# Kernel tuning notes

Measured on AMD Instinct MI355X. Metric: run time of the kernel, lower is better.

## Reference

```python
import jax, jax.numpy as jnp
import numpy as np


def _rnn_scan(x_tbi, h0, Wih, Whh, bih, bhh):
    # x_tbi: [T,B,I], h0: [B,H]. PyTorch nn.RNN cell: h = tanh(x@Wih^T + bih + h@Whh^T + bhh)
    def step(h, xt):
        h_new = jnp.tanh(xt @ Wih.T + bih + h @ Whh.T + bhh)
        return h_new, h_new
    h_last, hs = jax.lax.scan(step, h0, x_tbi)
    return h_last, hs


def setup_inputs() -> dict:
    key = jax.random.key(0)
    ks = jax.random.split(key, 12)
    B, T, I, H, O = 4096, 64, 3, 128, 3
    s = 1.0 / np.sqrt(H)
    d = {
        "x": jax.random.normal(ks[0], (B, T, I), dtype=jnp.float32),
        "enc_Wih": jax.random.uniform(ks[1], (H, I), jnp.float32, -s, s),
        "enc_Whh": jax.random.uniform(ks[2], (H, H), jnp.float32, -s, s),
        "enc_bih": jax.random.uniform(ks[3], (H,), jnp.float32, -s, s),
        "enc_bhh": jax.random.uniform(ks[4], (H,), jnp.float32, -s, s),
        "dec_Wih": jax.random.uniform(ks[5], (H, O), jnp.float32, -s, s),
        "dec_Whh": jax.random.uniform(ks[6], (H, H), jnp.float32, -s, s),
        "dec_bih": jax.random.uniform(ks[7], (H,), jnp.float32, -s, s),
        "dec_bhh": jax.random.uniform(ks[8], (H,), jnp.float32, -s, s),
        "fc_W": jax.random.uniform(ks[9], (O, H), jnp.float32, -s, s),
        "fc_b": jax.random.uniform(ks[10], (O,), jnp.float32, -s, s),
        "pred_len": 32,
    }
    return d


def reference(x, enc_Wih, enc_Whh, enc_bih, enc_bhh,
              dec_Wih, dec_Whh, dec_bih, dec_bhh, fc_W, fc_b, pred_len):
    B, T, _ = x.shape
    H = enc_Whh.shape[0]
    h0 = jnp.zeros((B, H), dtype=x.dtype)
    # Encoder over LOOK_BACK steps
    h, _ = _rnn_scan(jnp.swapaxes(x, 0, 1), h0, enc_Wih, enc_Whh, enc_bih, enc_bhh)
    dec_in0 = x[:, -1, :]  # [B,O]

    def step(carry, _):
        h, inp = carry
        h_new = jnp.tanh(inp @ dec_Wih.T + dec_bih + h @ dec_Whh.T + dec_bhh)
        pred = h_new @ fc_W.T + fc_b
        return (h_new, pred), pred

    _, preds = jax.lax.scan(step, (h, dec_in0), None, length=pred_len)
    out = jnp.swapaxes(preds, 0, 1)  # [B, pred_len, O]
    if pred_len == 1:
        return out[:, 0, :]
    return out
```

## Files before the change

kernel.cpp:

```cpp
#include <hip/hip_runtime.h>

typedef short short8 __attribute__((ext_vector_type(8)));
typedef float f32x4 __attribute__((ext_vector_type(4)));

#define H 128
#define NB 16
#define TSTEPS 64
#define PRED 32
#define XSTRIDE 260


static __device__ __forceinline__ unsigned short bf16_rne(float f) {
  unsigned u = __builtin_bit_cast(unsigned, f);
  u += 0x7fffu + ((u >> 16) & 1u);
  return (unsigned short)(u >> 16);
}
static __device__ __forceinline__ float bf16_f(unsigned short s) {
  unsigned u = ((unsigned)s) << 16;
  return __builtin_bit_cast(float, u);
}
static __device__ __forceinline__ float tanh_fast(float v) {
  v = fminf(9.0f, fmaxf(-9.0f, v));
  float e = __expf(2.0f * v);
  return __fdividef(e - 1.0f, e + 1.0f);
}

static __device__ __forceinline__ void split_frag(const f32x4& a, const f32x4& b,
                                                  short8& hi, short8& lo) {
  #pragma unroll
  for (int e = 0; e < 4; ++e) {
    unsigned short h1 = bf16_rne(a[e]);
    hi[e] = (short)h1;
    lo[e] = (short)bf16_rne(a[e] - bf16_f(h1));
    unsigned short h2 = bf16_rne(b[e]);
    hi[e + 4] = (short)h2;
    lo[e + 4] = (short)bf16_rne(b[e] - bf16_f(h2));
  }
}

__global__ __launch_bounds__(512, 2) void traj_kernel(
    const float* __restrict__ x,
    const float* __restrict__ eWih, const float* __restrict__ eWhh,
    const float* __restrict__ ebih, const float* __restrict__ ebhh,
    const float* __restrict__ dWih, const float* __restrict__ dWhh,
    const float* __restrict__ dbih, const float* __restrict__ dbhh,
    const float* __restrict__ fcW, const float* __restrict__ fcb,
    float* __restrict__ out)
{
  __shared__ __align__(16) float x_lds[NB * XSTRIDE];
  __shared__ __align__(16) short h_hi0[NB * H], h_lo0[NB * H];
  __shared__ __align__(16) short h_hi1[NB * H], h_lo1[NB * H];
  __shared__ float inp_lds[NB][4];

  const int tid = threadIdx.x;
  const int lane = tid & 63;
  const int w = tid >> 6;
  const int l4 = lane >> 4;
  const int ln = lane & 15;
  const int r0 = blockIdx.x * NB;
  const int jj = w * 16 + ln;

  #pragma unroll
  for (int s = 0; s < 6; ++s) {
    int flat = tid + s * 512;
    int r = flat / 192;
    int rem = flat - r * 192;
    int t = rem / 3;
    int i = rem - t * 3;
    x_lds[r * XSTRIDE + t * 4 + i] = x[(size_t)r0 * 192 + flat];
  }
  #pragma unroll
  for (int s = 0; s < 4; ++s) {
    h_hi0[tid + s * 512] = 0;
    h_lo0[tid + s * 512] = 0;
  }

  short8 whi[4], wlo[4];
  #pragma unroll
  for (int kt = 0; kt < 4; ++kt) {
    const float* p = eWhh + jj * H + kt * 32 + l4 * 8;
    split_frag(*(const f32x4*)p, *(const f32x4*)(p + 4), whi[kt], wlo[kt]);
  }
  float bias = ebih[jj] + ebhh[jj];
  float wi[3];
  #pragma unroll
  for (int i = 0; i < 3; ++i) wi[i] = eWih[jj * 3 + i];

  int roff[4];
  #pragma unroll
  for (int kt = 0; kt < 4; ++kt)
    roff[kt] = ln * H + ((((kt << 2) + l4) ^ ln) << 3);
  int wo[4], xb[4];
  #pragma unroll
  for (int reg = 0; reg < 4; ++reg) {
    const int r = l4 * 4 + reg;
    wo[reg] = r * H + (((jj >> 3) ^ r) << 3) + (jj & 7);
    xb[reg] = r * XSTRIDE;
  }

  auto load_frags = [&](const short* __restrict__ hh, const short* __restrict__ hl,
                        short8* ah, short8* al) {
    #pragma unroll
    for (int kt = 0; kt < 4; ++kt) {
      ah[kt] = *(const short8*)&hh[roff[kt]];
      al[kt] = *(const short8*)&hl[roff[kt]];
    }
  };
  auto rnn_core = [&](const short8* ah, const short8* al, f32x4 acc0,
                      short* __restrict__ wh, short* __restrict__ wl) {
    f32x4 accb = {0.f, 0.f, 0.f, 0.f};
    f32x4 accc = {0.f, 0.f, 0.f, 0.f};
    #pragma unroll
    for (int kt = 0; kt < 4; ++kt) {
      acc0 = __builtin_amdgcn_mfma_f32_16x16x32_bf16(ah[kt], whi[kt], acc0, 0, 0, 0);
      accb = __builtin_amdgcn_mfma_f32_16x16x32_bf16(ah[kt], wlo[kt], accb, 0, 0, 0);
      accc = __builtin_amdgcn_mfma_f32_16x16x32_bf16(al[kt], whi[kt], accc, 0, 0, 0);
    }
    #pragma unroll
    for (int reg = 0; reg < 4; ++reg) {
      float v = tanh_fast(acc0[reg] + accb[reg] + accc[reg]);
      unsigned short p = bf16_rne(v);
      wh[wo[reg]] = (short)p;
      wl[wo[reg]] = (short)bf16_rne(v - bf16_f(p));
    }
  };

  __syncthreads();

  for (int t = 0; t < TSTEPS; t += 2) {
    {
      short8 ah[4], al[4];
      load_frags(h_hi0, h_lo0, ah, al);
      f32x4 a;
      #pragma unroll
      for (int reg = 0; reg < 4; ++reg) {
        const f32x4 xv = *(const f32x4*)&x_lds[xb[reg] + t * 4];
        a[reg] = bias + wi[0] * xv[0] + wi[1] * xv[1] + wi[2] * xv[2];
      }
      rnn_core(ah, al, a, h_hi1, h_lo1);
    }
    __syncthreads();
    {
      short8 ah[4], al[4];
      load_frags(h_hi1, h_lo1, ah, al);
      f32x4 a;
      #pragma unroll
      for (int reg = 0; reg < 4; ++reg) {
        const f32x4 xv = *(const f32x4*)&x_lds[xb[reg] + (t + 1) * 4];
        a[reg] = bias + wi[0] * xv[0] + wi[1] * xv[1] + wi[2] * xv[2];
      }
      rnn_core(ah, al, a, h_hi0, h_lo0);
    }
    __syncthreads();
  }

  #pragma unroll
  for (int kt = 0; kt < 4; ++kt) {
    const float* p = dWhh + jj * H + kt * 32 + l4 * 8;
    split_frag(*(const f32x4*)p, *(const f32x4*)(p + 4), whi[kt], wlo[kt]);
  }
  bias = dbih[jj] + dbhh[jj];
  #pragma unroll
  for (int i = 0; i < 3; ++i) wi[i] = dWih[jj * 3 + i];

  short8 fhi[4];
  #pragma unroll
  for (int kt = 0; kt < 4; ++kt) {
    f32x4 a = {0.f, 0.f, 0.f, 0.f}, b = {0.f, 0.f, 0.f, 0.f};
    if (ln < 3) {
      const float* p = fcW + ln * H + kt * 32 + l4 * 8;
      a = *(const f32x4*)p;
      b = *(const f32x4*)(p + 4);
    }
    short8 hi;
    #pragma unroll
    for (int e = 0; e < 4; ++e) {
      hi[e] = (short)bf16_rne(a[e]);
      hi[e + 4] = (short)bf16_rne(b[e]);
    }
    fhi[kt] = hi;
  }
  const float fcbl = (ln < 3) ? fcb[ln] : 0.f;

  if (tid < 48) {
    int r = tid / 3, i = tid - 3 * (tid / 3);
    inp_lds[r][i] = x_lds[r * XSTRIDE + 63 * 4 + i];
  }
  __syncthreads();

  {
    short8 ah[4], al[4];
    load_frags(h_hi0, h_lo0, ah, al);
    f32x4 a;
    #pragma unroll
    for (int reg = 0; reg < 4; ++reg) {
      const int r = l4 * 4 + reg;
      a[reg] = bias + wi[0] * inp_lds[r][0] + wi[1] * inp_lds[r][1]
                    + wi[2] * inp_lds[r][2];
    }
    rnn_core(ah, al, a, h_hi1, h_lo1);
  }
  __syncthreads();

  #pragma unroll
  for (int kt = 0; kt < 4; ++kt) {
    const int kb = kt * 32 + l4 * 8;
    f32x4 a = *(const f32x4*)(dWhh + jj * H + kb);
    f32x4 b = *(const f32x4*)(dWhh + jj * H + kb + 4);
    #pragma unroll
    for (int o = 0; o < 3; ++o) {
      const f32x4 fa = *(const f32x4*)(fcW + o * H + kb);
      const f32x4 fb = *(const f32x4*)(fcW + o * H + kb + 4);
      #pragma unroll
      for (int e = 0; e < 4; ++e) {
        a[e] += wi[o] * fa[e];
        b[e] += wi[o] * fb[e];
      }
    }
    split_frag(a, b, whi[kt], wlo[kt]);
  }
  const float biasp = bias + wi[0] * fcb[0] + wi[1] * fcb[1] + wi[2] * fcb[2];
  const f32x4 accd = {biasp, biasp, biasp, biasp};

  const short* rdh = h_hi1; const short* rdl = h_lo1;
  short* wrh = h_hi0;       short* wrl = h_lo0;
  for (int s = 1; s < PRED; ++s) {
    short8 ah[4], al[4];
    load_frags(rdh, rdl, ah, al);
    rnn_core(ah, al, accd, wrh, wrl);
    if (w == (s & 7)) {
      f32x4 f0 = {0.f, 0.f, 0.f, 0.f};
      f32x4 f1 = {0.f, 0.f, 0.f, 0.f};
      #pragma unroll
      for (int kt = 0; kt < 4; ++kt) {
        f0 = __builtin_amdgcn_mfma_f32_16x16x32_bf16(ah[kt], fhi[kt], f0, 0, 0, 0);
        f1 = __builtin_amdgcn_mfma_f32_16x16x32_bf16(al[kt], fhi[kt], f1, 0, 0, 0);
      }
      if (ln < 3) {
        #pragma unroll
        for (int reg = 0; reg < 4; ++reg)
          out[((size_t)(r0 + l4 * 4 + reg) * PRED + (s - 1)) * 3 + ln] =
              f0[reg] + f1[reg] + fcbl;
      }
    }
    __syncthreads();
    const short* th = rdh; rdh = wrh; wrh = (short*)th;
    const short* tl = rdl; rdl = wrl; wrl = (short*)tl;
  }
  if (w == 0) {
    short8 ah[4], al[4];
    load_frags(rdh, rdl, ah, al);
    f32x4 f0 = {0.f, 0.f, 0.f, 0.f};
    f32x4 f1 = {0.f, 0.f, 0.f, 0.f};
    #pragma unroll
    for (int kt = 0; kt < 4; ++kt) {
      f0 = __builtin_amdgcn_mfma_f32_16x16x32_bf16(ah[kt], fhi[kt], f0, 0, 0, 0);
      f1 = __builtin_amdgcn_mfma_f32_16x16x32_bf16(al[kt], fhi[kt], f1, 0, 0, 0);
    }
    if (ln < 3) {
      #pragma unroll
      for (int reg = 0; reg < 4; ++reg)
        out[((size_t)(r0 + l4 * 4 + reg) * PRED + (PRED - 1)) * 3 + ln] =
            f0[reg] + f1[reg] + fcbl;
    }
  }
}

extern "C" void kernel_launch(void* const* d_in, const int* in_sizes, int n_in,
                              void* d_out, int out_size, void* d_ws, size_t ws_size,
                              hipStream_t stream) {
  (void)in_sizes; (void)n_in; (void)out_size; (void)d_ws; (void)ws_size;
  const float* x    = (const float*)d_in[0];
  const float* eWih = (const float*)d_in[1];
  const float* eWhh = (const float*)d_in[2];
  const float* ebih = (const float*)d_in[3];
  const float* ebhh = (const float*)d_in[4];
  const float* dWih = (const float*)d_in[5];
  const float* dWhh = (const float*)d_in[6];
  const float* dbih = (const float*)d_in[7];
  const float* dbhh = (const float*)d_in[8];
  const float* fcW  = (const float*)d_in[9];
  const float* fcb  = (const float*)d_in[10];
  float* out = (float*)d_out;
  traj_kernel<<<dim3(256), dim3(512), 0, stream>>>(
      x, eWih, eWhh, ebih, ebhh, dWih, dWhh, dbih, dbhh, fcW, fcb, out);
}
```

Baseline: 151.4 us.

## Halve batch rows per block and give each wave two output column tiles

Result: slower. 167.0 us (+10.3%).

```diff
diff --git a/kernel.cpp b/kernel.cpp
--- a/kernel.cpp
+++ b/kernel.cpp
@@ -4,7 +4,7 @@
 typedef float f32x4 __attribute__((ext_vector_type(4)));
 
 #define H 128
-#define NB 16
+#define NB 8
 #define TSTEPS 64
 #define PRED 32
 #define XSTRIDE 260
@@ -38,7 +38,7 @@
   }
 }
 
-__global__ __launch_bounds__(512, 2) void traj_kernel(
+__global__ __launch_bounds__(256, 2) void traj_kernel(
     const float* __restrict__ x,
     const float* __restrict__ eWih, const float* __restrict__ eWhh,
     const float* __restrict__ ebih, const float* __restrict__ ebhh,
@@ -47,10 +47,10 @@
     const float* __restrict__ fcW, const float* __restrict__ fcb,
     float* __restrict__ out)
 {
-  __shared__ __align__(16) float x_lds[NB * XSTRIDE];
-  __shared__ __align__(16) short h_hi0[NB * H], h_lo0[NB * H];
-  __shared__ __align__(16) short h_hi1[NB * H], h_lo1[NB * H];
-  __shared__ float inp_lds[NB][4];
+  __shared__ __align__(16) float x_lds[16 * XSTRIDE];
+  __shared__ __align__(16) short h_hi0[16 * H], h_lo0[16 * H];
+  __shared__ __align__(16) short h_hi1[16 * H], h_lo1[16 * H];
+  __shared__ float inp_lds[16][4];
 
   const int tid = threadIdx.x;
   const int lane = tid & 63;
@@ -58,43 +58,51 @@
   const int l4 = lane >> 4;
   const int ln = lane & 15;
   const int r0 = blockIdx.x * NB;
-  const int jj = w * 16 + ln;
-
-  #pragma unroll
-  for (int s = 0; s < 6; ++s) {
-    int flat = tid + s * 512;
+  const int jj0 = w * 32 + ln;
+  const int jj1 = jj0 + 16;
+
+  #pragma unroll
+  for (int s = 0; s < 12; ++s) {
+    int flat = tid + s * 256;
     int r = flat / 192;
     int rem = flat - r * 192;
     int t = rem / 3;
     int i = rem - t * 3;
-    x_lds[r * XSTRIDE + t * 4 + i] = x[(size_t)r0 * 192 + flat];
-  }
-  #pragma unroll
-  for (int s = 0; s < 4; ++s) {
-    h_hi0[tid + s * 512] = 0;
-    h_lo0[tid + s * 512] = 0;
-  }
-
-  short8 whi[4], wlo[4];
-  #pragma unroll
-  for (int kt = 0; kt < 4; ++kt) {
-    const float* p = eWhh + jj * H + kt * 32 + l4 * 8;
-    split_frag(*(const f32x4*)p, *(const f32x4*)(p + 4), whi[kt], wlo[kt]);
-  }
-  float bias = ebih[jj] + ebhh[jj];
-  float wi[3];
-  #pragma unroll
-  for (int i = 0; i < 3; ++i) wi[i] = eWih[jj * 3 + i];
+    int g = (r >> 2) * 2 + (r & 1);
+    x_lds[r * XSTRIDE + t * 4 + i] = x[(size_t)(r0 + g) * 192 + rem];
+  }
+  #pragma unroll
+  for (int s = 0; s < 8; ++s) {
+    h_hi0[tid + s * 256] = 0; h_hi1[tid + s * 256] = 0;
+    h_lo0[tid + s * 256] = 0; h_lo1[tid + s * 256] = 0;
+  }
+
+  short8 whi[2][4], wlo[2][4];
+  #pragma unroll
+  for (int ct = 0; ct < 2; ++ct) {
+    const int j = ct ? jj1 : jj0;
+    #pragma unroll
+    for (int kt = 0; kt < 4; ++kt) {
+      const float* p = eWhh + j * H + kt * 32 + l4 * 8;
+      split_frag(*(const f32x4*)p, *(const f32x4*)(p + 4), whi[ct][kt], wlo[ct][kt]);
+    }
+  }
+  float bias0 = ebih[jj0] + ebhh[jj0];
+  float bias1 = ebih[jj1] + ebhh[jj1];
+  float wi0[3], wi1[3];
+  #pragma unroll
+  for (int i = 0; i < 3; ++i) { wi0[i] = eWih[jj0 * 3 + i]; wi1[i] = eWih[jj1 * 3 + i]; }
 
   int roff[4];
   #pragma unroll
   for (int kt = 0; kt < 4; ++kt)
     roff[kt] = ln * H + ((((kt << 2) + l4) ^ ln) << 3);
-  int wo[4], xb[4];
-  #pragma unroll
-  for (int reg = 0; reg < 4; ++reg) {
+  int wo0[2], wo1[2], xb[2];
+  #pragma unroll
+  for (int reg = 0; reg < 2; ++reg) {
     const int r = l4 * 4 + reg;
-    wo[reg] = r * H + (((jj >> 3) ^ r) << 3) + (jj & 7);
+    wo0[reg] = r * H + (((jj0 >> 3) ^ r) << 3) + (jj0 & 7);
+    wo1[reg] = r * H + (((jj1 >> 3) ^ r) << 3) + (jj1 & 7);
     xb[reg] = r * XSTRIDE;
   }
 
@@ -106,22 +114,29 @@
       al[kt] = *(const short8*)&hl[roff[kt]];
     }
   };
-  auto rnn_core = [&](const short8* ah, const short8* al, f32x4 acc0,
+  auto rnn_core = [&](const short8* ah, const short8* al, f32x4 a0, f32x4 a1,
                       short* __restrict__ wh, short* __restrict__ wl) {
-    f32x4 accb = {0.f, 0.f, 0.f, 0.f};
-    f32x4 accc = {0.f, 0.f, 0.f, 0.f};
-    #pragma unroll
-    for (int kt = 0; kt < 4; ++kt) {
-      acc0 = __builtin_amdgcn_mfma_f32_16x16x32_bf16(ah[kt], whi[kt], acc0, 0, 0, 0);
-      accb = __builtin_amdgcn_mfma_f32_16x16x32_bf16(ah[kt], wlo[kt], accb, 0, 0, 0);
-      accc = __builtin_amdgcn_mfma_f32_16x16x32_bf16(al[kt], whi[kt], accc, 0, 0, 0);
-    }
-    #pragma unroll
-    for (int reg = 0; reg < 4; ++reg) {
-      float v = tanh_fast(acc0[reg] + accb[reg] + accc[reg]);
-      unsigned short p = bf16_rne(v);
-      wh[wo[reg]] = (short)p;
-      wl[wo[reg]] = (short)bf16_rne(v - bf16_f(p));
+    f32x4 b0 = {0.f, 0.f, 0.f, 0.f}, b1 = {0.f, 0.f, 0.f, 0.f};
+    f32x4 c0 = {0.f, 0.f, 0.f, 0.f}, c1 = {0.f, 0.f, 0.f, 0.f};
+    #pragma unroll
+    for (int kt = 0; kt < 4; ++kt) {
+      a0 = __builtin_amdgcn_mfma_f32_16x16x32_bf16(ah[kt], whi[0][kt], a0, 0, 0, 0);
+      a1 = __builtin_amdgcn_mfma_f32_16x16x32_bf16(ah[kt], whi[1][kt], a1, 0, 0, 0);
+      b0 = __builtin_amdgcn_mfma_f32_16x16x32_bf16(ah[kt], wlo[0][kt], b0, 0, 0, 0);
+      b1 = __builtin_amdgcn_mfma_f32_16x16x32_bf16(ah[kt], wlo[1][kt], b1, 0, 0, 0);
+      c0 = __builtin_amdgcn_mfma_f32_16x16x32_bf16(al[kt], whi[0][kt], c0, 0, 0, 0);
+      c1 = __builtin_amdgcn_mfma_f32_16x16x32_bf16(al[kt], whi[1][kt], c1, 0, 0, 0);
+    }
+    #pragma unroll
+    for (int reg = 0; reg < 2; ++reg) {
+      float v0 = tanh_fast(a0[reg] + b0[reg] + c0[reg]);
+      float v1 = tanh_fast(a1[reg] + b1[reg] + c1[reg]);
+      unsigned short p0 = bf16_rne(v0);
+      unsigned short p1 = bf16_rne(v1);
+      wh[wo0[reg]] = (short)p0;
+      wl[wo0[reg]] = (short)bf16_rne(v0 - bf16_f(p0));
+      wh[wo1[reg]] = (short)p1;
+      wl[wo1[reg]] = (short)bf16_rne(v1 - bf16_f(p1));
     }
   };
 
@@ -131,37 +146,44 @@
     {
       short8 ah[4], al[4];
       load_frags(h_hi0, h_lo0, ah, al);
-      f32x4 a;
-      #pragma unroll
-      for (int reg = 0; reg < 4; ++reg) {
+      f32x4 a0 = {0.f, 0.f, bias0, bias0}, a1 = {0.f, 0.f, bias1, bias1};
+      #pragma unroll
+      for (int reg = 0; reg < 2; ++reg) {
         const f32x4 xv = *(const f32x4*)&x_lds[xb[reg] + t * 4];
-        a[reg] = bias + wi[0] * xv[0] + wi[1] * xv[1] + wi[2] * xv[2];
-      }
-      rnn_core(ah, al, a, h_hi1, h_lo1);
+        a0[reg] = bias0 + wi0[0] * xv[0] + wi0[1] * xv[1] + wi0[2] * xv[2];
+        a1[reg] = bias1 + wi1[0] * xv[0] + wi1[1] * xv[1] + wi1[2] * xv[2];
+      }
+      rnn_core(ah, al, a0, a1, h_hi1, h_lo1);
     }
     __syncthreads();
     {
       short8 ah[4], al[4];
       load_frags(h_hi1, h_lo1, ah, al);
-      f32x4 a;
-      #pragma unroll
-      for (int reg = 0; reg < 4; ++reg) {
+      f32x4 a0 = {0.f, 0.f, bias0, bias0}, a1 = {0.f, 0.f, bias1, bias1};
+      #pragma unroll
+      for (int reg = 0; reg < 2; ++reg) {
         const f32x4 xv = *(const f32x4*)&x_lds[xb[reg] + (t + 1) * 4];
-        a[reg] = bias + wi[0] * xv[0] + wi[1] * xv[1] + wi[2] * xv[2];
-      }
-      rnn_core(ah, al, a, h_hi0, h_lo0);
+        a0[reg] = bias0 + wi0[0] * xv[0] + wi0[1] * xv[1] + wi0[2] * xv[2];
+        a1[reg] = bias1 + wi1[0] * xv[0] + wi1[1] * xv[1] + wi1[2] * xv[2];
+      }
+      rnn_core(ah, al, a0, a1, h_hi0, h_lo0);
     }
     __syncthreads();
   }
 
   #pragma unroll
-  for (int kt = 0; kt < 4; ++kt) {
-    const float* p = dWhh + jj * H + kt * 32 + l4 * 8;
-    split_frag(*(const f32x4*)p, *(const f32x4*)(p + 4), whi[kt], wlo[kt]);
-  }
-  bias = dbih[jj] + dbhh[jj];
-  #pragma unroll
-  for (int i = 0; i < 3; ++i) wi[i] = dWih[jj * 3 + i];
+  for (int ct = 0; ct < 2; ++ct) {
+    const int j = ct ? jj1 : jj0;
+    #pragma unroll
+    for (int kt = 0; kt < 4; ++kt) {
+      const float* p = dWhh + j * H + kt * 32 + l4 * 8;
+      split_frag(*(const f32x4*)p, *(const f32x4*)(p + 4), whi[ct][kt], wlo[ct][kt]);
+    }
+  }
+  bias0 = dbih[jj0] + dbhh[jj0];
+  bias1 = dbih[jj1] + dbhh[jj1];
+  #pragma unroll
+  for (int i = 0; i < 3; ++i) { wi0[i] = dWih[jj0 * 3 + i]; wi1[i] = dWih[jj1 * 3 + i]; }
 
   short8 fhi[4];
   #pragma unroll
@@ -191,56 +213,65 @@
   {
     short8 ah[4], al[4];
     load_frags(h_hi0, h_lo0, ah, al);
-    f32x4 a;
-    #pragma unroll
-    for (int reg = 0; reg < 4; ++reg) {
+    f32x4 a0 = {0.f, 0.f, bias0, bias0}, a1 = {0.f, 0.f, bias1, bias1};
+    #pragma unroll
+    for (int reg = 0; reg < 2; ++reg) {
       const int r = l4 * 4 + reg;
-      a[reg] = bias + wi[0] * inp_lds[r][0] + wi[1] * inp_lds[r][1]
-                    + wi[2] * inp_lds[r][2];
-    }
-    rnn_core(ah, al, a, h_hi1, h_lo1);
+      a0[reg] = bias0 + wi0[0] * inp_lds[r][0] + wi0[1] * inp_lds[r][1]
+                      + wi0[2] * inp_lds[r][2];
+      a1[reg] = bias1 + wi1[0] * inp_lds[r][0] + wi1[1] * inp_lds[r][1]
+                      + wi1[2] * inp_lds[r][2];
+    }
+    rnn_core(ah, al, a0, a1, h_hi1, h_lo1);
   }
   __syncthreads();
 
   #pragma unroll
-  for (int kt = 0; kt < 4; ++kt) {
-    const int kb = kt * 32 + l4 * 8;
-    f32x4 a = *(const f32x4*)(dWhh + jj * H + kb);
-    f32x4 b = *(const f32x4*)(dWhh + jj * H + kb + 4);
-    #pragma unroll
-    for (int o = 0; o < 3; ++o) {
-      const f32x4 fa = *(const f32x4*)(fcW + o * H + kb);
-      const f32x4 fb = *(const f32x4*)(fcW + o * H + kb + 4);
-      #pragma unroll
-      for (int e = 0; e < 4; ++e) {
-        a[e] += wi[o] * fa[e];
-        b[e] += wi[o] * fb[e];
-      }
-    }
-    split_frag(a, b, whi[kt], wlo[kt]);
-  }
-  const float biasp = bias + wi[0] * fcb[0] + wi[1] * fcb[1] + wi[2] * fcb[2];
-  const f32x4 accd = {biasp, biasp, biasp, biasp};
+  for (int ct = 0; ct < 2; ++ct) {
+    const int j = ct ? jj1 : jj0;
+    const float* wip = ct ? wi1 : wi0;
+    #pragma unroll
+    for (int kt = 0; kt < 4; ++kt) {
+      const int kb = kt * 32 + l4 * 8;
+      f32x4 a = *(const f32x4*)(dWhh + j * H + kb);
+      f32x4 b = *(const f32x4*)(dWhh + j * H + kb + 4);
+      #pragma unroll
+      for (int o = 0; o < 3; ++o) {
+        const f32x4 fa = *(const f32x4*)(fcW + o * H + kb);
+        const f32x4 fb = *(const f32x4*)(fcW + o * H + kb + 4);
+        #pragma unroll
+        for (int e = 0; e < 4; ++e) {
+          a[e] += wip[o] * fa[e];
+          b[e] += wip[o] * fb[e];
+        }
+      }
+      split_frag(a, b, whi[ct][kt], wlo[ct][kt]);
+    }
+  }
+  const float biasp0 = bias0 + wi0[0] * fcb[0] + wi0[1] * fcb[1] + wi0[2] * fcb[2];
+  const float biasp1 = bias1 + wi1[0] * fcb[0] + wi1[1] * fcb[1] + wi1[2] * fcb[2];
+  const f32x4 accd0 = {biasp0, biasp0, biasp0, biasp0};
+  const f32x4 accd1 = {biasp1, biasp1, biasp1, biasp1};
 
   const short* rdh = h_hi1; const short* rdl = h_lo1;
   short* wrh = h_hi0;       short* wrl = h_lo0;
   for (int s = 1; s < PRED; ++s) {
     short8 ah[4], al[4];
     load_frags(rdh, rdl, ah, al);
-    rnn_core(ah, al, accd, wrh, wrl);
-    if (w == (s & 7)) {
-      f32x4 f0 = {0.f, 0.f, 0.f, 0.f};
-      f32x4 f1 = {0.f, 0.f, 0.f, 0.f};
+    rnn_core(ah, al, accd0, accd1, wrh, wrl);
+    if (w == (s & 3)) {
+      f32x4 p0 = {0.f, 0.f, 0.f, 0.f};
+      f32x4 p1 = {0.f, 0.f, 0.f, 0.f};
       #pragma unroll
       for (int kt = 0; kt < 4; ++kt) {
-        f0 = __builtin_amdgcn_mfma_f32_16x16x32_bf16(ah[kt], fhi[kt], f0, 0, 0, 0);
-        f1 = __builtin_amdgcn_mfma_f32_16x16x32_bf16(al[kt], fhi[kt], f1, 0, 0, 0);
+        p0 = __builtin_amdgcn_mfma_f32_16x16x32_bf16(ah[kt], fhi[kt], p0, 0, 0, 0);
+        p1 = __builtin_amdgcn_mfma_f32_16x16x32_bf16(al[kt], fhi[kt], p1, 0, 0, 0);
       }
       if (ln < 3) {
         #pragma unroll
-        for (int reg = 0; reg < 4; ++reg)
-          out[((size_t)(r0 + l4 * 4 + reg) * PRED + (s - 1)) * 3 + ln] =
-              f0[reg] + f1[reg] + fcbl;
+        for (int reg = 0; reg < 2; ++reg)
+          out[((size_t)(r0 + l4 * 2 + reg) * PRED + (s - 1)) * 3 + ln] =
+              p0[reg] + p1[reg] + fcbl;
       }
     }
     __syncthreads();
@@ -250,18 +281,18 @@
   if (w == 0) {
     short8 ah[4], al[4];
     load_frags(rdh, rdl, ah, al);
-    f32x4 f0 = {0.f, 0.f, 0.f, 0.f};
-    f32x4 f1 = {0.f, 0.f, 0.f, 0.f};
-    #pragma unroll
-    for (int kt = 0; kt < 4; ++kt) {
-      f0 = __builtin_amdgcn_mfma_f32_16x16x32_bf16(ah[kt], fhi[kt], f0, 0, 0, 0);
-      f1 = __builtin_amdgcn_mfma_f32_16x16x32_bf16(al[kt], fhi[kt], f1, 0, 0, 0);
+    f32x4 p0 = {0.f, 0.f, 0.f, 0.f};
+    f32x4 p1 = {0.f, 0.f, 0.f, 0.f};
+    #pragma unroll
+    for (int kt = 0; kt < 4; ++kt) {
+      p0 = __builtin_amdgcn_mfma_f32_16x16x32_bf16(ah[kt], fhi[kt], p0, 0, 0, 0);
+      p1 = __builtin_amdgcn_mfma_f32_16x16x32_bf16(al[kt], fhi[kt], p1, 0, 0, 0);
     }
     if (ln < 3) {
       #pragma unroll
-      for (int reg = 0; reg < 4; ++reg)
-        out[((size_t)(r0 + l4 * 4 + reg) * PRED + (PRED - 1)) * 3 + ln] =
-            f0[reg] + f1[reg] + fcbl;
+      for (int reg = 0; reg < 2; ++reg)
+        out[((size_t)(r0 + l4 * 2 + reg) * PRED + (PRED - 1)) * 3 + ln] =
+            p0[reg] + p1[reg] + fcbl;
     }
   }
 }
@@ -282,6 +313,6 @@
   const float* fcW  = (const float*)d_in[9];
   const float* fcb  = (const float*)d_in[10];
   float* out = (float*)d_out;
-  traj_kernel<<<dim3(256), dim3(512), 0, stream>>>(
+  traj_kernel<<<dim3(512), dim3(256), 0, stream>>>(
       x, eWih, eWhh, ebih, ebhh, dWih, dWhh, dbih, dbhh, fcW, fcb, out);
 }
```

## Drop low-half hidden state split and stream x from global registers

Applied to the files above, without the earlier changes.

Result: faster. 136.9 us (-9.6%).

```diff
diff --git a/kernel.cpp b/kernel.cpp
--- a/kernel.cpp
+++ b/kernel.cpp
@@ -7,7 +7,6 @@
 #define NB 16
 #define TSTEPS 64
 #define PRED 32
-#define XSTRIDE 260
 
 
 static __device__ __forceinline__ unsigned short bf16_rne(float f) {
@@ -47,10 +46,8 @@
     const float* __restrict__ fcW, const float* __restrict__ fcb,
     float* __restrict__ out)
 {
-  __shared__ __align__(16) float x_lds[NB * XSTRIDE];
-  __shared__ __align__(16) short h_hi0[NB * H], h_lo0[NB * H];
-  __shared__ __align__(16) short h_hi1[NB * H], h_lo1[NB * H];
-  __shared__ float inp_lds[NB][4];
+  __shared__ __align__(16) short h_hi0[NB * H];
+  __shared__ __align__(16) short h_hi1[NB * H];
 
   const int tid = threadIdx.x;
   const int lane = tid & 63;
@@ -61,19 +58,8 @@
   const int jj = w * 16 + ln;
 
   #pragma unroll
-  for (int s = 0; s < 6; ++s) {
-    int flat = tid + s * 512;
-    int r = flat / 192;
-    int rem = flat - r * 192;
-    int t = rem / 3;
-    int i = rem - t * 3;
-    x_lds[r * XSTRIDE + t * 4 + i] = x[(size_t)r0 * 192 + flat];
-  }
-  #pragma unroll
-  for (int s = 0; s < 4; ++s) {
+  for (int s = 0; s < 4; ++s)
     h_hi0[tid + s * 512] = 0;
-    h_lo0[tid + s * 512] = 0;
-  }
 
   short8 whi[4], wlo[4];
   #pragma unroll
@@ -90,68 +76,72 @@
   #pragma unroll
   for (int kt = 0; kt < 4; ++kt)
     roff[kt] = ln * H + ((((kt << 2) + l4) ^ ln) << 3);
-  int wo[4], xb[4];
+  int wo[4];
+  const float* xrow[4];
   #pragma unroll
   for (int reg = 0; reg < 4; ++reg) {
     const int r = l4 * 4 + reg;
     wo[reg] = r * H + (((jj >> 3) ^ r) << 3) + (jj & 7);
-    xb[reg] = r * XSTRIDE;
-  }
-
-  auto load_frags = [&](const short* __restrict__ hh, const short* __restrict__ hl,
-                        short8* ah, short8* al) {
-    #pragma unroll
-    for (int kt = 0; kt < 4; ++kt) {
+    xrow[reg] = x + (size_t)(r0 + r) * 192;
+  }
+
+  auto load_frags = [&](const short* __restrict__ hh, short8* ah) {
+    #pragma unroll
+    for (int kt = 0; kt < 4; ++kt)
       ah[kt] = *(const short8*)&hh[roff[kt]];
-      al[kt] = *(const short8*)&hl[roff[kt]];
-    }
   };
-  auto rnn_core = [&](const short8* ah, const short8* al, f32x4 acc0,
-                      short* __restrict__ wh, short* __restrict__ wl) {
+  auto rnn_core = [&](const short8* ah, f32x4 acc0, short* __restrict__ wh) {
     f32x4 accb = {0.f, 0.f, 0.f, 0.f};
-    f32x4 accc = {0.f, 0.f, 0.f, 0.f};
     #pragma unroll
     for (int kt = 0; kt < 4; ++kt) {
       acc0 = __builtin_amdgcn_mfma_f32_16x16x32_bf16(ah[kt], whi[kt], acc0, 0, 0, 0);
       accb = __builtin_amdgcn_mfma_f32_16x16x32_bf16(ah[kt], wlo[kt], accb, 0, 0, 0);
-      accc = __builtin_amdgcn_mfma_f32_16x16x32_bf16(al[kt], whi[kt], accc, 0, 0, 0);
     }
     #pragma unroll
     for (int reg = 0; reg < 4; ++reg) {
-      float v = tanh_fast(acc0[reg] + accb[reg] + accc[reg]);
-      unsigned short p = bf16_rne(v);
-      wh[wo[reg]] = (short)p;
-      wl[wo[reg]] = (short)bf16_rne(v - bf16_f(p));
+      float v = tanh_fast(acc0[reg] + accb[reg]);
+      wh[wo[reg]] = (short)bf16_rne(v);
     }
   };
+
+  float xc[4][3], xn[4][3];
+  #pragma unroll
+  for (int reg = 0; reg < 4; ++reg)
+    #pragma unroll
+    for (int i = 0; i < 3; ++i) xc[reg][i] = xrow[reg][i];
 
   __syncthreads();
 
   for (int t = 0; t < TSTEPS; t += 2) {
     {
-      short8 ah[4], al[4];
-      load_frags(h_hi0, h_lo0, ah, al);
+      short8 ah[4];
+      load_frags(h_hi0, ah);
       f32x4 a;
       #pragma unroll
-      for (int reg = 0; reg < 4; ++reg) {
-        const f32x4 xv = *(const f32x4*)&x_lds[xb[reg] + t * 4];
-        a[reg] = bias + wi[0] * xv[0] + wi[1] * xv[1] + wi[2] * xv[2];
-      }
-      rnn_core(ah, al, a, h_hi1, h_lo1);
-    }
-    __syncthreads();
+      for (int reg = 0; reg < 4; ++reg)
+        a[reg] = bias + wi[0] * xc[reg][0] + wi[1] * xc[reg][1] + wi[2] * xc[reg][2];
+      #pragma unroll
+      for (int reg = 0; reg < 4; ++reg)
+        #pragma unroll
+        for (int i = 0; i < 3; ++i) xn[reg][i] = xrow[reg][(t + 1) * 3 + i];
+      rnn_core(ah, a, h_hi1);
+      __syncthreads();
+    }
     {
-      short8 ah[4], al[4];
-      load_frags(h_hi1, h_lo1, ah, al);
+      short8 ah[4];
+      load_frags(h_hi1, ah);
       f32x4 a;
       #pragma unroll
-      for (int reg = 0; reg < 4; ++reg) {
-        const f32x4 xv = *(const f32x4*)&x_lds[xb[reg] + (t + 1) * 4];
-        a[reg] = bias + wi[0] * xv[0] + wi[1] * xv[1] + wi[2] * xv[2];
-      }
-      rnn_core(ah, al, a, h_hi0, h_lo0);
-    }
-    __syncthreads();
+      for (int reg = 0; reg < 4; ++reg)
+        a[reg] = bias + wi[0] * xn[reg][0] + wi[1] * xn[reg][1] + wi[2] * xn[reg][2];
+      const int tp = (t + 2 < TSTEPS) ? (t + 2) : (TSTEPS - 1);
+      #pragma unroll
+      for (int reg = 0; reg < 4; ++reg)
+        #pragma unroll
+        for (int i = 0; i < 3; ++i) xc[reg][i] = xrow[reg][tp * 3 + i];
+      rnn_core(ah, a, h_hi0);
+      __syncthreads();
+    }
   }
 
   #pragma unroll
@@ -182,23 +172,14 @@
   }
   const float fcbl = (ln < 3) ? fcb[ln] : 0.f;
 
-  if (tid < 48) {
-    int r = tid / 3, i = tid - 3 * (tid / 3);
-    inp_lds[r][i] = x_lds[r * XSTRIDE + 63 * 4 + i];
-  }
-  __syncthreads();
-
   {
-    short8 ah[4], al[4];
-    load_frags(h_hi0, h_lo0, ah, al);
+    short8 ah[4];
+    load_frags(h_hi0, ah);
     f32x4 a;
     #pragma unroll
-    for (int reg = 0; reg < 4; ++reg) {
-      const int r = l4 * 4 + reg;
-      a[reg] = bias + wi[0] * inp_lds[r][0] + wi[1] * inp_lds[r][1]
-                    + wi[2] * inp_lds[r][2];
-    }
-    rnn_core(ah, al, a, h_hi1, h_lo1);
+    for (int reg = 0; reg < 4; ++reg)
+      a[reg] = bias + wi[0] * xc[reg][0] + wi[1] * xc[reg][1] + wi[2] * xc[reg][2];
+    rnn_core(ah, a, h_hi1);
   }
   __syncthreads();
 
@@ -222,46 +203,39 @@
   const float biasp = bias + wi[0] * fcb[0] + wi[1] * fcb[1] + wi[2] * fcb[2];
   const f32x4 accd = {biasp, biasp, biasp, biasp};
 
-  const short* rdh = h_hi1; const short* rdl = h_lo1;
-  short* wrh = h_hi0;       short* wrl = h_lo0;
+  const short* rdh = h_hi1;
+  short* wrh = h_hi0;
   for (int s = 1; s < PRED; ++s) {
-    short8 ah[4], al[4];
-    load_frags(rdh, rdl, ah, al);
-    rnn_core(ah, al, accd, wrh, wrl);
+    short8 ah[4];
+    load_frags(rdh, ah);
+    rnn_core(ah, accd, wrh);
     if (w == (s & 7)) {
-      f32x4 f0 = {0.f, 0.f, 0.f, 0.f};
-      f32x4 f1 = {0.f, 0.f, 0.f, 0.f};
-      #pragma unroll
-      for (int kt = 0; kt < 4; ++kt) {
-        f0 = __builtin_amdgcn_mfma_f32_16x16x32_bf16(ah[kt], fhi[kt], f0, 0, 0, 0);
-        f1 = __builtin_amdgcn_mfma_f32_16x16x32_bf16(al[kt], fhi[kt], f1, 0, 0, 0);
-      }
+      f32x4 p0 = {0.f, 0.f, 0.f, 0.f};
+      #pragma unroll
+      for (int kt = 0; kt < 4; ++kt)
+        p0 = __builtin_amdgcn_mfma_f32_16x16x32_bf16(ah[kt], fhi[kt], p0, 0, 0, 0);
       if (ln < 3) {
         #pragma unroll
         for (int reg = 0; reg < 4; ++reg)
           out[((size_t)(r0 + l4 * 4 + reg) * PRED + (s - 1)) * 3 + ln] =
-              f0[reg] + f1[reg] + fcbl;
+              p0[reg] + fcbl;
       }
     }
     __syncthreads();
     const short* th = rdh; rdh = wrh; wrh = (short*)th;
-    const short* tl = rdl; rdl = wrl; wrl = (short*)tl;
   }
   if (w == 0) {
-    short8 ah[4], al[4];
-    load_frags(rdh, rdl, ah, al);
-    f32x4 f0 = {0.f, 0.f, 0.f, 0.f};
-    f32x4 f1 = {0.f, 0.f, 0.f, 0.f};
-    #pragma unroll
-    for (int kt = 0; kt < 4; ++kt) {
-      f0 = __builtin_amdgcn_mfma_f32_16x16x32_bf16(ah[kt], fhi[kt], f0, 0, 0, 0);
-      f1 = __builtin_amdgcn_mfma_f32_16x16x32_bf16(al[kt], fhi[kt], f1, 0, 0, 0);
-    }
+    short8 ah[4];
+    load_frags(rdh, ah);
+    f32x4 p0 = {0.f, 0.f, 0.f, 0.f};
+    #pragma unroll
+    for (int kt = 0; kt < 4; ++kt)
+      p0 = __builtin_amdgcn_mfma_f32_16x16x32_bf16(ah[kt], fhi[kt], p0, 0, 0, 0);
     if (ln < 3) {
       #pragma unroll
       for (int reg = 0; reg < 4; ++reg)
         out[((size_t)(r0 + l4 * 4 + reg) * PRED + (PRED - 1)) * 3 + ln] =
-            f0[reg] + f1[reg] + fcbl;
+            p0[reg] + fcbl;
     }
   }
 }
```
